# Kernel tuning notes

Measured on AMD Instinct MI355X. Metric: run time of the kernel, lower is better.

The kernel has to match this reference:

```python
import jax, jax.numpy as jnp
import numpy as np
from math import sqrt

N = 8192      # points
I = 16        # in_channels
H = 64        # hidden_units
O = 64        # out_channels
CUTS = 8      # conv MLP intermediate width
RADIUS = 9.0
GROUPS = 4    # GroupNorm groups
BLK = 128     # i-block size for tiled pairwise reduction (KeOps-style)


def _leaky(x):
    return jnp.where(x >= 0, x, 0.2 * x)


def _group_norm(f, w, b, eps=1e-5):
    # torch GroupNorm applied to (1, C, N): stats per group over (C//G channels x N points)
    n, c = f.shape
    g = f.reshape(n, GROUPS, c // GROUPS)
    m = g.mean(axis=(0, 2), keepdims=True)
    v = ((g - m) ** 2).mean(axis=(0, 2), keepdims=True)
    g = (g - m) * jax.lax.rsqrt(v + eps)
    return g.reshape(n, c) * w + b


def setup_inputs() -> dict:
    key = jax.random.key(0)
    ks = jax.random.split(key, 20)
    U = lambda k, s, lim: jax.random.uniform(k, s, minval=-lim, maxval=lim)
    points = jax.random.normal(ks[0], (N, 3), dtype=jnp.float32)
    nuv = jax.random.normal(ks[1], (N, 3, 3), dtype=jnp.float32)
    features = jax.random.normal(ks[2], (N, I), dtype=jnp.float32)
    # net_in (torch Linear default init)
    W_in1 = U(ks[3], (H, I), 1 / np.sqrt(I)); b_in1 = U(ks[4], (H,), 1 / np.sqrt(I))
    W_in2 = U(ks[5], (H, H), 1 / np.sqrt(H)); b_in2 = U(ks[6], (H,), 1 / np.sqrt(H))
    # conv MLP with custom init from the module
    A1 = jax.random.normal(ks[7], (CUTS, 3), dtype=jnp.float32)
    B1 = jax.random.uniform(ks[8], (CUTS,)) * 0.8 * jnp.sqrt((A1 ** 2).sum(-1))
    A2 = U(ks[9], (H, CUTS), 1 / np.sqrt(CUTS))
    B2 = jax.random.normal(ks[10], (H,)) * 0.5 * jnp.sqrt((A2 ** 2).sum(-1))
    # net_out
    W_out1 = U(ks[11], (O, H), 1 / np.sqrt(H)); b_out1 = U(ks[12], (O,), 1 / np.sqrt(H))
    W_out2 = U(ks[13], (O, O), 1 / np.sqrt(O)); b_out2 = U(ks[14], (O,), 1 / np.sqrt(O))
    return {
        "points": points, "nuv": nuv, "features": features,
        "W_in1": W_in1, "b_in1": b_in1, "W_in2": W_in2, "b_in2": b_in2,
        "gn_in_w": jnp.ones((H,), jnp.float32), "gn_in_b": jnp.zeros((H,), jnp.float32),
        "A1": A1, "B1": B1, "A2": A2, "B2": B2,
        "W_out1": W_out1, "b_out1": b_out1, "W_out2": W_out2, "b_out2": b_out2,
        "gn_out_w": jnp.ones((O,), jnp.float32), "gn_out_b": jnp.zeros((O,), jnp.float32),
    }


def _forward(points, nuv, features, W_in1, b_in1, W_in2, b_in2, gn_in_w, gn_in_b,
             A1, B1, A2, B2, W_out1, b_out1, W_out2, b_out2, gn_out_w, gn_out_b):
    # 1. net_in + GroupNorm
    f = _leaky(features @ W_in1.T + b_in1)
    f = _leaky(f @ W_in2.T + b_in2)
    f = _group_norm(f, gn_in_w, gn_in_b)          # (N, H)
    # 2. quasi-geodesic interaction, tiled over i-blocks (KeOps-style)
    pts = points / (sqrt(2.0) * RADIUS)
    normals = jax.lax.stop_gradient(nuv[:, 0, :])  # n_j is detached in the original
    nblk = N // BLK

    def body(carry, blk):
        xi, nuvi = blk                              # (B,3), (B,3,3)
        ni = nuvi[:, 0, :]                          # (B,3) n_i (not detached)
        diff = pts[None, :, :] - xi[:, None, :]     # (B,N,3) x_j - x_i
        dn = ni @ normals.T                         # (B,N) <n_i, n_j>
        d2 = (diff ** 2).sum(-1) * (2.0 - dn) ** 2  # pseudo-geodesic squared dist
        w = jnp.exp(-d2)                            # Gaussian window
        X = jnp.einsum('bij,bnj->bni', nuvi, diff)  # coords in local basis (B,N,3)
        h = jax.nn.relu(jnp.einsum('bnj,cj->bnc', X, A1) + B1)   # (B,N,CUTS)
        g = jax.nn.relu(jnp.einsum('bnc,hc->bnh', h, A2) + B2)   # (B,N,H)
        out = jnp.einsum('bn,bnh,nh->bh', w, g, f)  # sum_j w_ij * conv(P_ij) * f_j
        return carry, out

    _, outs = jax.lax.scan(
        body, None, (pts.reshape(nblk, BLK, 3), nuv.reshape(nblk, BLK, 3, 3)))
    f2 = outs.reshape(N, H)
    # 3. net_out + GroupNorm
    f2 = _leaky(f2 @ W_out1.T + b_out1)
    f2 = _leaky(f2 @ W_out2.T + b_out2)
    f2 = _group_norm(f2, gn_out_w, gn_out_b)       # (N, O)
    return f2


def reference(points, nuv, features, W_in1, b_in1, W_in2, b_in2, gn_in_w, gn_in_b,
              A1, B1, A2, B2, W_out1, b_out1, W_out2, b_out2, gn_out_w, gn_out_b):
    return _forward(points, nuv, features, W_in1, b_in1, W_in2, b_in2, gn_in_w, gn_in_b,
                    A1, B1, A2, B2, W_out1, b_out1, W_out2, b_out2, gn_out_w, gn_out_b)
```

## Files before the change

kernel.cpp:

```cpp
#include <hip/hip_runtime.h>
#include <hip/hip_bf16.h>
#include <stdint.h>


#define N_PTS   8192
#define CHUNK   64
#define NCHUNK  (N_PTS / CHUNK)
#define WPB     8
#define PSCALE  0.07856742013183861f
#define GN_CNT  (N_PTS * 16)
#define FS_STRIDE 76
#define CHUNK_FLOATS (CHUNK * FS_STRIDE)

#define OFF_POINTS 0
#define OFF_NUV    24576
#define OFF_FEAT   98304
#define OFF_WIN1   229376
#define OFF_BIN1   230400
#define OFF_WIN2   230464
#define OFF_BIN2   234560
#define OFF_GNIW   234624
#define OFF_GNIB   234688
#define OFF_A1     234752
#define OFF_B1     234776
#define OFF_A2     234784
#define OFF_B2     235296
#define OFF_WOUT1  235360
#define OFF_BOUT1  239456
#define OFF_WOUT2  239520
#define OFF_BOUT2  243616
#define OFF_GNOW   243680
#define OFF_GNOB   243744
#define CVT_TOTAL  243808
#define NSEG 19

typedef _Float16 half2_t __attribute__((ext_vector_type(2)));
typedef _Float16 f16x8   __attribute__((ext_vector_type(8)));
typedef float    f32x4   __attribute__((ext_vector_type(4)));
typedef __attribute__((address_space(3))) uint32_t lds_u32_t;
typedef __attribute__((address_space(1))) const uint32_t glb_u32_t;

struct InPtrs { const void* p[NSEG]; };

__device__ __forceinline__ float rfl(float x) {
  return __int_as_float(__builtin_amdgcn_readfirstlane(__float_as_int(x)));
}
__device__ __forceinline__ float leaky(float x) { return x > 0.f ? x : 0.2f * x; }

#if __has_builtin(__builtin_amdgcn_cvt_pkrtz)
__device__ __forceinline__ half2_t pk16(float a, float b) {
  return __builtin_bit_cast(half2_t, __builtin_amdgcn_cvt_pkrtz(a, b));
}
#else
__device__ __forceinline__ half2_t pk16(float a, float b) {
  half2_t r; r.x = (_Float16)a; r.y = (_Float16)b; return r;
}
#endif

__global__ __launch_bounds__(256) void prep_kernel(InPtrs ptrs, float* dst,
                                                   float* gstats) {
  if (blockIdx.x == 0 && threadIdx.x < 16) gstats[threadIdx.x] = 0.f;
  const uint32_t w0 = ((const uint32_t*)ptrs.p[7])[0];
  const bool bf = (w0 != 0x3F800000u);
  const int CUM[NSEG + 1] = {0, 24576, 98304, 229376, 230400, 230464, 234560,
                             234624, 234688, 234752, 234776, 234784, 235296,
                             235360, 239456, 239520, 243616, 243680, 243744,
                             243808};
  for (int e = blockIdx.x * 256 + threadIdx.x; e < CVT_TOTAL;
       e += gridDim.x * 256) {
    int s = 0;
#pragma unroll
    for (int i = 1; i < NSEG; ++i) s += (e >= CUM[i]) ? 1 : 0;
    const int rem = e - CUM[s];
    float v = bf ? __bfloat162float(((const __hip_bfloat16*)ptrs.p[s])[rem])
                 : ((const float*)ptrs.p[s])[rem];
    if (s == 0) v *= PSCALE;
    dst[e] = v;
  }
}

__global__ __launch_bounds__(256) void mlp_in_kernel(
    const float* __restrict__ pool, float* __restrict__ fbuf,
    float* __restrict__ gstats) {
  __shared__ float ls[4][64];
  __shared__ float red[8];
  const int t = threadIdx.x, nl = t >> 6, h = t & 63;
  const int n = blockIdx.x * 4 + nl;
  const float4* fr = (const float4*)(pool + OFF_FEAT + n * 16);
  const float4* w1 = (const float4*)(pool + OFF_WIN1 + h * 16);
  float a = pool[OFF_BIN1 + h];
#pragma unroll
  for (int k = 0; k < 4; ++k) {
    const float4 x = fr[k], w = w1[k];
    a = fmaf(x.x, w.x, a); a = fmaf(x.y, w.y, a);
    a = fmaf(x.z, w.z, a); a = fmaf(x.w, w.w, a);
  }
  if (t < 8) red[t] = 0.f;
  ls[nl][h] = leaky(a);
  __syncthreads();
  const float4* w2 = (const float4*)(pool + OFF_WIN2 + h * 64);
  const float4* lr = (const float4*)&ls[nl][0];
  float c = pool[OFF_BIN2 + h];
#pragma unroll
  for (int k = 0; k < 16; ++k) {
    const float4 x = lr[k], w = w2[k];
    c = fmaf(x.x, w.x, c); c = fmaf(x.y, w.y, c);
    c = fmaf(x.z, w.z, c); c = fmaf(x.w, w.w, c);
  }
  c = leaky(c);
  fbuf[n * 64 + h] = c;
  float s = c, q = c * c;
#pragma unroll
  for (int off = 8; off; off >>= 1) { s += __shfl_xor(s, off); q += __shfl_xor(q, off); }
  if ((h & 15) == 0) { atomicAdd(&red[h >> 4], s); atomicAdd(&red[4 + (h >> 4)], q); }
  __syncthreads();
  if (t < 8) atomicAdd(&gstats[t], red[t]);
}

__global__ __launch_bounds__(256) void mlp_out_kernel(
    const float* __restrict__ cbuf, const float* __restrict__ pool,
    float* __restrict__ obuf, float* __restrict__ gstats) {
  __shared__ float ls[4][64];
  __shared__ float red[8];
  const int t = threadIdx.x, nl = t >> 6, h = t & 63;
  const int n = blockIdx.x * 4 + nl;
  const float4* cr = (const float4*)(cbuf + n * 64);
  const float4* w1 = (const float4*)(pool + OFF_WOUT1 + h * 64);
  float a = pool[OFF_BOUT1 + h];
#pragma unroll
  for (int k = 0; k < 16; ++k) {
    const float4 x = cr[k], w = w1[k];
    a = fmaf(x.x, w.x, a); a = fmaf(x.y, w.y, a);
    a = fmaf(x.z, w.z, a); a = fmaf(x.w, w.w, a);
  }
  if (t < 8) red[t] = 0.f;
  ls[nl][h] = leaky(a);
  __syncthreads();
  const float4* w2 = (const float4*)(pool + OFF_WOUT2 + h * 64);
  const float4* lr = (const float4*)&ls[nl][0];
  float c = pool[OFF_BOUT2 + h];
#pragma unroll
  for (int k = 0; k < 16; ++k) {
    const float4 x = lr[k], w = w2[k];
    c = fmaf(x.x, w.x, c); c = fmaf(x.y, w.y, c);
    c = fmaf(x.z, w.z, c); c = fmaf(x.w, w.w, c);
  }
  c = leaky(c);
  obuf[n * 64 + h] = c;
  float s = c, q = c * c;
#pragma unroll
  for (int off = 8; off; off >>= 1) { s += __shfl_xor(s, off); q += __shfl_xor(q, off); }
  if ((h & 15) == 0) { atomicAdd(&red[h >> 4], s); atomicAdd(&red[4 + (h >> 4)], q); }
  __syncthreads();
  if (t < 8) atomicAdd(&gstats[t], red[t]);
}

__global__ __launch_bounds__(256) void gn_apply_pad_kernel(
    const float* __restrict__ buf, const float* __restrict__ gstats,
    const float* __restrict__ pool, float* __restrict__ fpad) {
  const int idx = blockIdx.x * 256 + threadIdx.x;
  const int h = idx & 63, n = idx >> 6, g = h >> 4;
  const float m = gstats[g] * (1.f / GN_CNT);
  const float v = gstats[4 + g] * (1.f / GN_CNT) - m * m;
  const float rs = rsqrtf(fmaxf(v, 0.f) + 1e-5f);
  const float r = fmaf((buf[idx] - m) * rs, pool[OFF_GNIW + h], pool[OFF_GNIB + h]);
  fpad[(n >> 6) * CHUNK_FLOATS + h * FS_STRIDE + (n & 63)] = r;
}

__global__ __launch_bounds__(256) void gn_apply_out_kernel(
    const float* __restrict__ buf, const float* __restrict__ gstats,
    const float* __restrict__ pool, void* __restrict__ out,
    const uint32_t* __restrict__ dref) {
  const bool bf = (dref[0] != 0x3F800000u);
  const int idx = blockIdx.x * 256 + threadIdx.x;
  const int h = idx & 63, g = h >> 4;
  const float m = gstats[g] * (1.f / GN_CNT);
  const float v = gstats[4 + g] * (1.f / GN_CNT) - m * m;
  const float rs = rsqrtf(fmaxf(v, 0.f) + 1e-5f);
  const float r = fmaf((buf[idx] - m) * rs, pool[OFF_GNOW + h], pool[OFF_GNOB + h]);
  if (bf) ((__hip_bfloat16*)out)[idx] = __float2bfloat16(r);
  else    ((float*)out)[idx] = r;
}

__global__ __launch_bounds__(512, 4) void conv_kernel(
    const float* __restrict__ pool, const float* __restrict__ fpad,
    float* __restrict__ cbuf) {
  __shared__ float  f_s[CHUNK_FLOATS];
  __shared__ float4 hcA[WPB][2][4][33];

  const int t = threadIdx.x;
  const int wv = t >> 6, lane = t & 63;
  const int b0 = blockIdx.x * WPB + wv;
  const int b1 = b0 + N_PTS / 2;
  const int kg  = lane >> 4;
  const int l15 = lane & 15;
  const int idx_fp = (kg < 2) ? (kg * 16 + l15) : 32;

  const float p0x = rfl(pool[OFF_POINTS + b0 * 3 + 0]);
  const float p0y = rfl(pool[OFF_POINTS + b0 * 3 + 1]);
  const float p0z = rfl(pool[OFF_POINTS + b0 * 3 + 2]);
  const float p1x = rfl(pool[OFF_POINTS + b1 * 3 + 0]);
  const float p1y = rfl(pool[OFF_POINTS + b1 * 3 + 1]);
  const float p1z = rfl(pool[OFF_POINTS + b1 * 3 + 2]);
  float nb0[9], nb1[9];
#pragma unroll
  for (int i = 0; i < 9; ++i) nb0[i] = rfl(pool[OFF_NUV + b0 * 9 + i]);
#pragma unroll
  for (int i = 0; i < 9; ++i) nb1[i] = rfl(pool[OFF_NUV + b1 * 9 + i]);
  float a1v[24], b1v[8];
#pragma unroll
  for (int i = 0; i < 24; ++i) a1v[i] = rfl(pool[OFF_A1 + i]);
#pragma unroll
  for (int i = 0; i < 8; ++i)  b1v[i] = rfl(pool[OFF_B1 + i]);

  f16x8 bfrag[4];
#pragma unroll
  for (int ht = 0; ht < 4; ++ht) {
    const int h = 16 * ht + l15;
#pragma unroll
    for (int i = 0; i < 8; ++i) {
      float v = 0.f;
      if (kg == 0) v = pool[OFF_A2 + h * 8 + i];
      else if (kg == 1 && i == 0) v = pool[OFF_B2 + h];
      bfrag[ht][i] = (_Float16)v;
    }
  }

  if (lane < 17) {
    float4 z4; z4.x = 0.f; z4.y = 0.f; z4.z = 0.f; z4.w = 0.f;
#pragma unroll
    for (int jt = 0; jt < 4; ++jt) {
      hcA[wv][0][jt][16 + lane] = z4;
      hcA[wv][1][jt][16 + lane] = z4;
    }
  }

  const f32x4 kzero = {0.f, 0.f, 0.f, 0.f};
  float acc0[4] = {0.f, 0.f, 0.f, 0.f};
  float acc1[4] = {0.f, 0.f, 0.f, 0.f};

  for (int c = 0; c < NCHUNK; ++c) {
    const int n = c * CHUNK + lane;
    const float px = pool[OFF_POINTS + n * 3 + 0];
    const float py = pool[OFF_POINTS + n * 3 + 1];
    const float pz = pool[OFF_POINTS + n * 3 + 2];
    const float nx = pool[OFF_NUV + n * 9 + 0];
    const float ny = pool[OFF_NUV + n * 9 + 1];
    const float nz = pool[OFF_NUV + n * 9 + 2];

    __syncthreads();

    {
      const glb_u32_t* src = (const glb_u32_t*)(fpad + c * CHUNK_FLOATS);
      lds_u32_t* dst = (lds_u32_t*)f_s;
      __builtin_amdgcn_global_load_lds(src + t * 4, dst + t * 4, 16, 0, 0);
      __builtin_amdgcn_global_load_lds(src + 2048 + t * 4, dst + 2048 + t * 4,
                                       16, 0, 0);
      if (t < 192)
        __builtin_amdgcn_global_load_lds(src + 4096 + t * 4,
                                         dst + 4096 + t * 4, 16, 0, 0);
    }

    {
      const float dx = px - p0x, dy = py - p0y, dz = pz - p0z;
      const float X0 = fmaf(nb0[0], dx, fmaf(nb0[1], dy, nb0[2] * dz));
      const float X1 = fmaf(nb0[3], dx, fmaf(nb0[4], dy, nb0[5] * dz));
      const float X2 = fmaf(nb0[6], dx, fmaf(nb0[7], dy, nb0[8] * dz));
      const float dn = fmaf(nb0[0], nx, fmaf(nb0[1], ny, nb0[2] * nz));
      const float dd = fmaf(dx, dx, fmaf(dy, dy, dz * dz));
      const float tt = 2.f - dn;
      const float w = __expf(-dd * tt * tt);
      float hc[8];
#pragma unroll
      for (int cc = 0; cc < 8; ++cc)
        hc[cc] = w * fmaxf(fmaf(X0, a1v[cc * 3 + 0],
                           fmaf(X1, a1v[cc * 3 + 1],
                           fmaf(X2, a1v[cc * 3 + 2], b1v[cc]))), 0.f);
      float4 lo;
      lo.x = __builtin_bit_cast(float, pk16(hc[0], hc[1]));
      lo.y = __builtin_bit_cast(float, pk16(hc[2], hc[3]));
      lo.z = __builtin_bit_cast(float, pk16(hc[4], hc[5]));
      lo.w = __builtin_bit_cast(float, pk16(hc[6], hc[7]));
      hcA[wv][0][lane >> 4][l15] = lo;
      ((float*)&hcA[wv][0][lane >> 4][16 + l15])[0] =
          __builtin_bit_cast(float, pk16(w, 0.f));
    }
    {
      const float dx = px - p1x, dy = py - p1y, dz = pz - p1z;
      const float X0 = fmaf(nb1[0], dx, fmaf(nb1[1], dy, nb1[2] * dz));
      const float X1 = fmaf(nb1[3], dx, fmaf(nb1[4], dy, nb1[5] * dz));
      const float X2 = fmaf(nb1[6], dx, fmaf(nb1[7], dy, nb1[8] * dz));
      const float dn = fmaf(nb1[0], nx, fmaf(nb1[1], ny, nb1[2] * nz));
      const float dd = fmaf(dx, dx, fmaf(dy, dy, dz * dz));
      const float tt = 2.f - dn;
      const float w = __expf(-dd * tt * tt);
      float hc[8];
#pragma unroll
      for (int cc = 0; cc < 8; ++cc)
        hc[cc] = w * fmaxf(fmaf(X0, a1v[cc * 3 + 0],
                           fmaf(X1, a1v[cc * 3 + 1],
                           fmaf(X2, a1v[cc * 3 + 2], b1v[cc]))), 0.f);
      float4 lo;
      lo.x = __builtin_bit_cast(float, pk16(hc[0], hc[1]));
      lo.y = __builtin_bit_cast(float, pk16(hc[2], hc[3]));
      lo.z = __builtin_bit_cast(float, pk16(hc[4], hc[5]));
      lo.w = __builtin_bit_cast(float, pk16(hc[6], hc[7]));
      hcA[wv][1][lane >> 4][l15] = lo;
      ((float*)&hcA[wv][1][lane >> 4][16 + l15])[0] =
          __builtin_bit_cast(float, pk16(w, 0.f));
    }

    __syncthreads();

#pragma unroll
    for (int jt = 0; jt < 4; ++jt) {
      const f16x8 af0 = __builtin_bit_cast(f16x8, hcA[wv][0][jt][idx_fp]);
      const f16x8 af1 = __builtin_bit_cast(f16x8, hcA[wv][1][jt][idx_fp]);
      const int nbase = 16 * jt + 4 * kg;
#pragma unroll
      for (int ht = 0; ht < 4; ++ht) {
        const f32x4 D0 = __builtin_amdgcn_mfma_f32_16x16x32_f16(
            af0, bfrag[ht], kzero, 0, 0, 0);
        const f32x4 D1 = __builtin_amdgcn_mfma_f32_16x16x32_f16(
            af1, bfrag[ht], kzero, 0, 0, 0);
        const float4 fq = *(const float4*)
            &f_s[(16 * ht + l15) * FS_STRIDE + nbase];
        acc0[ht] = fmaf(fq.x, fmaxf(D0[0], 0.f), acc0[ht]);
        acc0[ht] = fmaf(fq.y, fmaxf(D0[1], 0.f), acc0[ht]);
        acc0[ht] = fmaf(fq.z, fmaxf(D0[2], 0.f), acc0[ht]);
        acc0[ht] = fmaf(fq.w, fmaxf(D0[3], 0.f), acc0[ht]);
        acc1[ht] = fmaf(fq.x, fmaxf(D1[0], 0.f), acc1[ht]);
        acc1[ht] = fmaf(fq.y, fmaxf(D1[1], 0.f), acc1[ht]);
        acc1[ht] = fmaf(fq.z, fmaxf(D1[2], 0.f), acc1[ht]);
        acc1[ht] = fmaf(fq.w, fmaxf(D1[3], 0.f), acc1[ht]);
      }
    }
  }

#pragma unroll
  for (int ht = 0; ht < 4; ++ht) {
    acc0[ht] += __shfl_xor(acc0[ht], 16, 64);
    acc0[ht] += __shfl_xor(acc0[ht], 32, 64);
    acc1[ht] += __shfl_xor(acc1[ht], 16, 64);
    acc1[ht] += __shfl_xor(acc1[ht], 32, 64);
  }
  if (lane < 16) {
#pragma unroll
    for (int ht = 0; ht < 4; ++ht) {
      cbuf[b0 * 64 + 16 * ht + lane] = acc0[ht];
      cbuf[b1 * 64 + 16 * ht + lane] = acc1[ht];
    }
  }
}

extern "C" void kernel_launch(void* const* d_in, const int* in_sizes, int n_in,
                              void* d_out, int out_size, void* d_ws, size_t ws_size,
                              hipStream_t stream) {
  (void)in_sizes; (void)n_in; (void)out_size; (void)ws_size;
  const uint32_t* dref = (const uint32_t*)d_in[7];

  float* pool   = (float*)d_ws;
  float* fbuf   = pool + CVT_TOTAL;
  float* fpad   = fbuf + N_PTS * 64;
  float* cbuf   = fpad + NCHUNK * CHUNK_FLOATS;
  float* gstats = cbuf + N_PTS * 64;

  InPtrs ptrs;
  for (int i = 0; i < NSEG; ++i) ptrs.p[i] = d_in[i];

  prep_kernel<<<256, 256, 0, stream>>>(ptrs, pool, gstats);
  mlp_in_kernel<<<N_PTS / 4, 256, 0, stream>>>(pool, fbuf, gstats);
  gn_apply_pad_kernel<<<N_PTS * 64 / 256, 256, 0, stream>>>(fbuf, gstats, pool,
                                                            fpad);
  conv_kernel<<<N_PTS / 2 / WPB, 512, 0, stream>>>(pool, fpad, cbuf);
  mlp_out_kernel<<<N_PTS / 4, 256, 0, stream>>>(cbuf, pool, fbuf, gstats + 8);
  gn_apply_out_kernel<<<N_PTS * 64 / 256, 256, 0, stream>>>(
      fbuf, gstats + 8, pool, d_out, dref);
}
```

Measured before the change: 726.9 us.

## Widen conv chunk to 128 points with point-major feature tile and fewer barriers

The conv kernel now stages 128 source points per iteration instead of 64, using a point-major padded layout for the normalized features (stride 68), written that way by the GN pad kernel. Each iteration runs two 64-point sub-steps behind a single block barrier, relying on each wave owning its own hcA slot, which halves barrier count and global-load issue overhead. In exchange LDS per block grows and the minimum-blocks launch bound is dropped, which lowers occupancy. Feature reads become four scalar LDS loads instead of one float4, with possible bank conflicts.

```diff
diff --git a/kernel.cpp b/kernel.cpp
--- a/kernel.cpp
+++ b/kernel.cpp
@@ -4,13 +4,12 @@
 
 
 #define N_PTS   8192
-#define CHUNK   64
-#define NCHUNK  (N_PTS / CHUNK)
+#define NCH2    64
 #define WPB     8
 #define PSCALE  0.07856742013183861f
 #define GN_CNT  (N_PTS * 16)
-#define FS_STRIDE 76
-#define CHUNK_FLOATS (CHUNK * FS_STRIDE)
+#define FS_STRIDE 68
+#define TILE_FLOATS (128 * FS_STRIDE)
 
 #define OFF_POINTS 0
 #define OFF_NUV    24576
@@ -164,7 +163,7 @@
   const float v = gstats[4 + g] * (1.f / GN_CNT) - m * m;
   const float rs = rsqrtf(fmaxf(v, 0.f) + 1e-5f);
   const float r = fmaf((buf[idx] - m) * rs, pool[OFF_GNIW + h], pool[OFF_GNIB + h]);
-  fpad[(n >> 6) * CHUNK_FLOATS + h * FS_STRIDE + (n & 63)] = r;
+  fpad[(n >> 7) * TILE_FLOATS + (n & 127) * FS_STRIDE + h] = r;
 }
 
 __global__ __launch_bounds__(256) void gn_apply_out_kernel(
@@ -182,10 +181,10 @@
   else    ((float*)out)[idx] = r;
 }
 
-__global__ __launch_bounds__(512, 4) void conv_kernel(
+__global__ __launch_bounds__(512) void conv_kernel(
     const float* __restrict__ pool, const float* __restrict__ fpad,
     float* __restrict__ cbuf) {
-  __shared__ float  f_s[CHUNK_FLOATS];
+  __shared__ float  f_s[TILE_FLOATS];
   __shared__ float4 hcA[WPB][2][4][33];
 
   const int t = threadIdx.x;
@@ -239,100 +238,104 @@
   float acc0[4] = {0.f, 0.f, 0.f, 0.f};
   float acc1[4] = {0.f, 0.f, 0.f, 0.f};
 
-  for (int c = 0; c < NCHUNK; ++c) {
-    const int n = c * CHUNK + lane;
-    const float px = pool[OFF_POINTS + n * 3 + 0];
-    const float py = pool[OFF_POINTS + n * 3 + 1];
-    const float pz = pool[OFF_POINTS + n * 3 + 2];
-    const float nx = pool[OFF_NUV + n * 9 + 0];
-    const float ny = pool[OFF_NUV + n * 9 + 1];
-    const float nz = pool[OFF_NUV + n * 9 + 2];
-
+  for (int c = 0; c < NCH2; ++c) {
     __syncthreads();
 
     {
-      const glb_u32_t* src = (const glb_u32_t*)(fpad + c * CHUNK_FLOATS);
+      const glb_u32_t* src = (const glb_u32_t*)(fpad + c * TILE_FLOATS);
       lds_u32_t* dst = (lds_u32_t*)f_s;
       __builtin_amdgcn_global_load_lds(src + t * 4, dst + t * 4, 16, 0, 0);
       __builtin_amdgcn_global_load_lds(src + 2048 + t * 4, dst + 2048 + t * 4,
                                        16, 0, 0);
-      if (t < 192)
-        __builtin_amdgcn_global_load_lds(src + 4096 + t * 4,
-                                         dst + 4096 + t * 4, 16, 0, 0);
-    }
-
-    {
-      const float dx = px - p0x, dy = py - p0y, dz = pz - p0z;
-      const float X0 = fmaf(nb0[0], dx, fmaf(nb0[1], dy, nb0[2] * dz));
-      const float X1 = fmaf(nb0[3], dx, fmaf(nb0[4], dy, nb0[5] * dz));
-      const float X2 = fmaf(nb0[6], dx, fmaf(nb0[7], dy, nb0[8] * dz));
-      const float dn = fmaf(nb0[0], nx, fmaf(nb0[1], ny, nb0[2] * nz));
-      const float dd = fmaf(dx, dx, fmaf(dy, dy, dz * dz));
-      const float tt = 2.f - dn;
-      const float w = __expf(-dd * tt * tt);
-      float hc[8];
-#pragma unroll
-      for (int cc = 0; cc < 8; ++cc)
-        hc[cc] = w * fmaxf(fmaf(X0, a1v[cc * 3 + 0],
-                           fmaf(X1, a1v[cc * 3 + 1],
-                           fmaf(X2, a1v[cc * 3 + 2], b1v[cc]))), 0.f);
-      float4 lo;
-      lo.x = __builtin_bit_cast(float, pk16(hc[0], hc[1]));
-      lo.y = __builtin_bit_cast(float, pk16(hc[2], hc[3]));
-      lo.z = __builtin_bit_cast(float, pk16(hc[4], hc[5]));
-      lo.w = __builtin_bit_cast(float, pk16(hc[6], hc[7]));
-      hcA[wv][0][lane >> 4][l15] = lo;
-      ((float*)&hcA[wv][0][lane >> 4][16 + l15])[0] =
-          __builtin_bit_cast(float, pk16(w, 0.f));
-    }
-    {
-      const float dx = px - p1x, dy = py - p1y, dz = pz - p1z;
-      const float X0 = fmaf(nb1[0], dx, fmaf(nb1[1], dy, nb1[2] * dz));
-      const float X1 = fmaf(nb1[3], dx, fmaf(nb1[4], dy, nb1[5] * dz));
-      const float X2 = fmaf(nb1[6], dx, fmaf(nb1[7], dy, nb1[8] * dz));
-      const float dn = fmaf(nb1[0], nx, fmaf(nb1[1], ny, nb1[2] * nz));
-      const float dd = fmaf(dx, dx, fmaf(dy, dy, dz * dz));
-      const float tt = 2.f - dn;
-      const float w = __expf(-dd * tt * tt);
-      float hc[8];
-#pragma unroll
-      for (int cc = 0; cc < 8; ++cc)
-        hc[cc] = w * fmaxf(fmaf(X0, a1v[cc * 3 + 0],
-                           fmaf(X1, a1v[cc * 3 + 1],
-                           fmaf(X2, a1v[cc * 3 + 2], b1v[cc]))), 0.f);
-      float4 lo;
-      lo.x = __builtin_bit_cast(float, pk16(hc[0], hc[1]));
-      lo.y = __builtin_bit_cast(float, pk16(hc[2], hc[3]));
-      lo.z = __builtin_bit_cast(float, pk16(hc[4], hc[5]));
-      lo.w = __builtin_bit_cast(float, pk16(hc[6], hc[7]));
-      hcA[wv][1][lane >> 4][l15] = lo;
-      ((float*)&hcA[wv][1][lane >> 4][16 + l15])[0] =
-          __builtin_bit_cast(float, pk16(w, 0.f));
-    }
-
-    __syncthreads();
-
-#pragma unroll
-    for (int jt = 0; jt < 4; ++jt) {
-      const f16x8 af0 = __builtin_bit_cast(f16x8, hcA[wv][0][jt][idx_fp]);
-      const f16x8 af1 = __builtin_bit_cast(f16x8, hcA[wv][1][jt][idx_fp]);
-      const int nbase = 16 * jt + 4 * kg;
-#pragma unroll
-      for (int ht = 0; ht < 4; ++ht) {
-        const f32x4 D0 = __builtin_amdgcn_mfma_f32_16x16x32_f16(
-            af0, bfrag[ht], kzero, 0, 0, 0);
-        const f32x4 D1 = __builtin_amdgcn_mfma_f32_16x16x32_f16(
-            af1, bfrag[ht], kzero, 0, 0, 0);
-        const float4 fq = *(const float4*)
-            &f_s[(16 * ht + l15) * FS_STRIDE + nbase];
-        acc0[ht] = fmaf(fq.x, fmaxf(D0[0], 0.f), acc0[ht]);
-        acc0[ht] = fmaf(fq.y, fmaxf(D0[1], 0.f), acc0[ht]);
-        acc0[ht] = fmaf(fq.z, fmaxf(D0[2], 0.f), acc0[ht]);
-        acc0[ht] = fmaf(fq.w, fmaxf(D0[3], 0.f), acc0[ht]);
-        acc1[ht] = fmaf(fq.x, fmaxf(D1[0], 0.f), acc1[ht]);
-        acc1[ht] = fmaf(fq.y, fmaxf(D1[1], 0.f), acc1[ht]);
-        acc1[ht] = fmaf(fq.z, fmaxf(D1[2], 0.f), acc1[ht]);
-        acc1[ht] = fmaf(fq.w, fmaxf(D1[3], 0.f), acc1[ht]);
+      __builtin_amdgcn_global_load_lds(src + 4096 + t * 4, dst + 4096 + t * 4,
+                                       16, 0, 0);
+      __builtin_amdgcn_global_load_lds(src + 6144 + t * 4, dst + 6144 + t * 4,
+                                       16, 0, 0);
+      if (t < 128)
+        __builtin_amdgcn_global_load_lds(src + 8192 + t * 4,
+                                         dst + 8192 + t * 4, 16, 0, 0);
+    }
+
+#pragma unroll
+    for (int s = 0; s < 2; ++s) {
+      const int n = c * 128 + s * 64 + lane;
+      const float px = pool[OFF_POINTS + n * 3 + 0];
+      const float py = pool[OFF_POINTS + n * 3 + 1];
+      const float pz = pool[OFF_POINTS + n * 3 + 2];
+      const float nx = pool[OFF_NUV + n * 9 + 0];
+      const float ny = pool[OFF_NUV + n * 9 + 1];
+      const float nz = pool[OFF_NUV + n * 9 + 2];
+      {
+        const float dx = px - p0x, dy = py - p0y, dz = pz - p0z;
+        const float X0 = fmaf(nb0[0], dx, fmaf(nb0[1], dy, nb0[2] * dz));
+        const float X1 = fmaf(nb0[3], dx, fmaf(nb0[4], dy, nb0[5] * dz));
+        const float X2 = fmaf(nb0[6], dx, fmaf(nb0[7], dy, nb0[8] * dz));
+        const float dn = fmaf(nb0[0], nx, fmaf(nb0[1], ny, nb0[2] * nz));
+        const float dd = fmaf(dx, dx, fmaf(dy, dy, dz * dz));
+        const float tt = 2.f - dn;
+        const float w = __expf(-dd * tt * tt);
+        float hc[8];
+#pragma unroll
+        for (int cc = 0; cc < 8; ++cc)
+          hc[cc] = w * fmaxf(fmaf(X0, a1v[cc * 3 + 0],
+                             fmaf(X1, a1v[cc * 3 + 1],
+                             fmaf(X2, a1v[cc * 3 + 2], b1v[cc]))), 0.f);
+        float4 lo;
+        lo.x = __builtin_bit_cast(float, pk16(hc[0], hc[1]));
+        lo.y = __builtin_bit_cast(float, pk16(hc[2], hc[3]));
+        lo.z = __builtin_bit_cast(float, pk16(hc[4], hc[5]));
+        lo.w = __builtin_bit_cast(float, pk16(hc[6], hc[7]));
+        hcA[wv][0][lane >> 4][l15] = lo;
+        ((float*)&hcA[wv][0][lane >> 4][16 + l15])[0] =
+            __builtin_bit_cast(float, pk16(w, 0.f));
+      }
+      {
+        const float dx = px - p1x, dy = py - p1y, dz = pz - p1z;
+        const float X0 = fmaf(nb1[0], dx, fmaf(nb1[1], dy, nb1[2] * dz));
+        const float X1 = fmaf(nb1[3], dx, fmaf(nb1[4], dy, nb1[5] * dz));
+        const float X2 = fmaf(nb1[6], dx, fmaf(nb1[7], dy, nb1[8] * dz));
+        const float dn = fmaf(nb1[0], nx, fmaf(nb1[1], ny, nb1[2] * nz));
+        const float dd = fmaf(dx, dx, fmaf(dy, dy, dz * dz));
+        const float tt = 2.f - dn;
+        const float w = __expf(-dd * tt * tt);
+        float hc[8];
+#pragma unroll
+        for (int cc = 0; cc < 8; ++cc)
+          hc[cc] = w * fmaxf(fmaf(X0, a1v[cc * 3 + 0],
+                             fmaf(X1, a1v[cc * 3 + 1],
+                             fmaf(X2, a1v[cc * 3 + 2], b1v[cc]))), 0.f);
+        float4 lo;
+        lo.x = __builtin_bit_cast(float, pk16(hc[0], hc[1]));
+        lo.y = __builtin_bit_cast(float, pk16(hc[2], hc[3]));
+        lo.z = __builtin_bit_cast(float, pk16(hc[4], hc[5]));
+        lo.w = __builtin_bit_cast(float, pk16(hc[6], hc[7]));
+        hcA[wv][1][lane >> 4][l15] = lo;
+        ((float*)&hcA[wv][1][lane >> 4][16 + l15])[0] =
+            __builtin_bit_cast(float, pk16(w, 0.f));
+      }
+
+      if (s == 0) __syncthreads();
+
+      const int srow = s * 64;
+#pragma unroll
+      for (int jt = 0; jt < 4; ++jt) {
+        const f16x8 af0 = __builtin_bit_cast(f16x8, hcA[wv][0][jt][idx_fp]);
+        const f16x8 af1 = __builtin_bit_cast(f16x8, hcA[wv][1][jt][idx_fp]);
+        const int fbase = (srow + 16 * jt + 4 * kg) * FS_STRIDE + l15;
+#pragma unroll
+        for (int ht = 0; ht < 4; ++ht) {
+          const f32x4 D0 = __builtin_amdgcn_mfma_f32_16x16x32_f16(
+              af0, bfrag[ht], kzero, 0, 0, 0);
+          const f32x4 D1 = __builtin_amdgcn_mfma_f32_16x16x32_f16(
+              af1, bfrag[ht], kzero, 0, 0, 0);
+          const float* fb = &f_s[fbase + 16 * ht];
+#pragma unroll
+          for (int r = 0; r < 4; ++r) {
+            const float fj = fb[r * FS_STRIDE];
+            acc0[ht] = fmaf(fj, fmaxf(D0[r], 0.f), acc0[ht]);
+            acc1[ht] = fmaf(fj, fmaxf(D1[r], 0.f), acc1[ht]);
+          }
+        }
       }
     }
   }
@@ -362,7 +365,7 @@
   float* pool   = (float*)d_ws;
   float* fbuf   = pool + CVT_TOTAL;
   float* fpad   = fbuf + N_PTS * 64;
-  float* cbuf   = fpad + NCHUNK * CHUNK_FLOATS;
+  float* cbuf   = fpad + NCH2 * TILE_FLOATS;
   float* gstats = cbuf + N_PTS * 64;
 
   InPtrs ptrs;
```

Result: slower. 784.3 us (+7.9%).
